# Kernel optimization log

Measured on AMD Instinct MI355X. Metric: run time of the kernel, lower is better.

The kernel has to match this reference:

```python
import jax, jax.numpy as jnp
import numpy as np

BIAS = 0.0001
TEMPERATURE = 1.0


def setup_inputs() -> dict:
    key = jax.random.key(0)
    k_h, k_w1, k_w2, k_u = jax.random.split(key, 4)
    N, H, Z = 8192, 64, 128
    h = jax.random.normal(k_h, (N, H), dtype=jnp.float32)
    W1 = jax.random.normal(k_w1, (H, H), dtype=jnp.float32) * (1.0 / np.sqrt(H))
    b1 = jnp.zeros((H,), dtype=jnp.float32)
    W2 = jax.random.normal(k_w2, (H, Z), dtype=jnp.float32) * (1.0 / np.sqrt(H))
    b2 = jnp.zeros((Z,), dtype=jnp.float32)
    noise_u = jax.random.uniform(k_u, (N, N), dtype=jnp.float32)
    return {"h": h, "W1": W1, "b1": b1, "W2": W2, "b2": b2, "noise_u": noise_u}


def reference(h, W1, b1, W2, b2, noise_u):
    # MLPA: Linear -> ReLU -> Linear, then outer-product adjacency logits
    Zmat = jnp.maximum(h @ W1 + b1, 0.0) @ W2 + b2          # [N, dim_z]
    adj_logits = Zmat @ Zmat.T                               # [N, N]
    # gumbel-sigmoid edge sampling (training path)
    eps = (2.0 * BIAS - 1.0) * noise_u + (1.0 - BIAS)        # uniform in [bias, 1-bias]
    gate = (jnp.log(eps) - jnp.log1p(-eps) + adj_logits) / TEMPERATURE
    adj = jax.nn.sigmoid(gate)
    # keep strict upper triangle, symmetrize
    adj = jnp.triu(adj, 1)
    adj = adj + adj.T
    # fill_diagonal_(1)
    N = adj.shape[0]
    idx = jnp.arange(N)
    adj = adj.at[idx, idx].set(1.0)
    # D^{-1/2} @ adj @ D^{-1/2} expressed as row/col rescale (same math)
    d = jnp.power(adj.sum(axis=1), -0.5)                     # [N]
    adj_norm = d[:, None] * adj * d[None, :]
    return adj_norm, adj_logits
```

## Files before the change

### kernel.cpp

```cpp
#include <hip/hip_runtime.h>
#include <hip/hip_bf16.h>
#include <math.h>

#define N 8192
#define ZD 128
#define NTILE 64
#define NUPPER 2080

typedef __attribute__((ext_vector_type(8))) _Float16 f16x8;
typedef __attribute__((ext_vector_type(4))) float f32x4;

__device__ __forceinline__ int tri_cum(int ti) {
    return (ti * (2 * NTILE + 1 - ti)) / 2;
}

__device__ __forceinline__ void tile_decode(int t, int& ti, int& tj) {
    int est = (int)((129.0f - sqrtf(16641.0f - 8.0f * (float)t)) * 0.5f);
    if (est < 0) est = 0;
    while (tri_cum(est) > t) --est;
    while (tri_cum(est + 1) <= t) ++est;
    ti = est;
    tj = est + (t - tri_cum(est));
}

__global__ __launch_bounds__(256) void k1_mlp(
    const float* __restrict__ h, const float* __restrict__ W1,
    const float* __restrict__ b1, const float* __restrict__ W2,
    const float* __restrict__ b2, _Float16* __restrict__ Zf,
    float* __restrict__ sums)
{
    __shared__ float W1s[64][65];
    __shared__ float W2s[64][129];
    __shared__ float hs[32][68];
    __shared__ float Ts[32][68];
    __shared__ float b1s[64];
    __shared__ float b2s[128];
    const int tid = threadIdx.x;
    const int row0 = blockIdx.x * 32;

    if (tid < 32) sums[row0 + tid] = 1.0f;

    for (int e = tid; e < 64 * 64; e += 256) W1s[e >> 6][e & 63] = W1[e];
    for (int e = tid; e < 64 * 128; e += 256) W2s[e >> 7][e & 127] = W2[e];
    for (int e = tid; e < 32 * 64; e += 256) hs[e >> 6][e & 63] = h[(size_t)row0 * 64 + e];
    if (tid < 64) b1s[tid] = b1[tid];
    if (tid < 128) b2s[tid] = b2[tid];
    __syncthreads();

    {
        const int c = tid & 63;
        const int r0 = (tid >> 6) * 8;
        float s[8];
        #pragma unroll
        for (int j = 0; j < 8; ++j) s[j] = b1s[c];
        #pragma unroll
        for (int k0 = 0; k0 < 64; k0 += 4) {
            const float w0 = W1s[k0 + 0][c], w1 = W1s[k0 + 1][c];
            const float w2 = W1s[k0 + 2][c], w3 = W1s[k0 + 3][c];
            #pragma unroll
            for (int j = 0; j < 8; ++j) {
                f32x4 hv = *(const f32x4*)&hs[r0 + j][k0];
                s[j] = fmaf(hv[0], w0, s[j]);
                s[j] = fmaf(hv[1], w1, s[j]);
                s[j] = fmaf(hv[2], w2, s[j]);
                s[j] = fmaf(hv[3], w3, s[j]);
            }
        }
        #pragma unroll
        for (int j = 0; j < 8; ++j) Ts[r0 + j][c] = fmaxf(s[j], 0.0f);
    }
    __syncthreads();

    {
        const int c = tid & 127;
        const int r0 = (tid >> 7) * 16;
        float s[16];
        #pragma unroll
        for (int j = 0; j < 16; ++j) s[j] = b2s[c];
        #pragma unroll
        for (int k0 = 0; k0 < 64; k0 += 4) {
            const float w0 = W2s[k0 + 0][c], w1 = W2s[k0 + 1][c];
            const float w2 = W2s[k0 + 2][c], w3 = W2s[k0 + 3][c];
            #pragma unroll
            for (int j = 0; j < 16; ++j) {
                f32x4 tv = *(const f32x4*)&Ts[r0 + j][k0];
                s[j] = fmaf(tv[0], w0, s[j]);
                s[j] = fmaf(tv[1], w1, s[j]);
                s[j] = fmaf(tv[2], w2, s[j]);
                s[j] = fmaf(tv[3], w3, s[j]);
            }
        }
        #pragma unroll
        for (int j = 0; j < 16; ++j)
            Zf[(size_t)(row0 + r0 + j) * ZD + c] = (_Float16)s[j];
    }
}

__global__ __launch_bounds__(256, 3) void k3_main(
    const _Float16* __restrict__ Zf, const float* __restrict__ noise,
    float* __restrict__ logits, unsigned char* __restrict__ vws,
    float* __restrict__ sums)
{
    int ti, tj;
    const int t = (blockIdx.x & 7) * (NUPPER / 8) + (blockIdx.x >> 3);
    tile_decode(t, ti, tj);
    const bool diag = (ti == tj);

    __shared__ float T[128][65];
    __shared__ float rs2[128][16];
    __shared__ float cs2[16][128];

    const int tid = threadIdx.x;
    const int lane = tid & 63;
    const int w = tid >> 6;
    const int wr = w >> 1, wc = w & 1;
    const int fr = lane & 15;
    const int kg = lane >> 4;
    const int i0 = ti * 128, j0 = tj * 128;

    unsigned char* __restrict__ vtile = vws + (size_t)t * (128 * 128);

    const _Float16* Ap = Zf + (size_t)(i0 + wr * 64) * ZD;
    const _Float16* Bp = Zf + (size_t)(j0 + wc * 64) * ZD;

    f32x4 acc[4][4];
    #pragma unroll
    for (int mf = 0; mf < 4; ++mf)
        #pragma unroll
        for (int nf = 0; nf < 4; ++nf)
            acc[mf][nf] = (f32x4)0.0f;

    #pragma unroll
    for (int kc = 0; kc < 4; ++kc) {
        const int ko = kc * 32 + kg * 8;
        f16x8 a[4], b[4];
        #pragma unroll
        for (int mf = 0; mf < 4; ++mf) {
            size_t off = (size_t)(mf * 16 + fr) * ZD + ko;
            a[mf] = *(const f16x8*)(Ap + off);
            b[mf] = *(const f16x8*)(Bp + off);
        }
        #pragma unroll
        for (int mf = 0; mf < 4; ++mf)
            #pragma unroll
            for (int nf = 0; nf < 4; ++nf)
                acc[mf][nf] = __builtin_amdgcn_mfma_f32_16x16x32_f16(a[mf], b[nf], acc[mf][nf], 0, 0, 0);
    }

    const int cid = tid & 15;
    const int c4 = cid * 4;
    const int rbase = tid >> 4;

    float rsacc[8];
    #pragma unroll
    for (int it = 0; it < 8; ++it) rsacc[it] = 0.0f;

    #pragma unroll
    for (int half = 0; half < 2; ++half) {
        __syncthreads();
        if (wc == half) {
            #pragma unroll
            for (int mf = 0; mf < 4; ++mf)
                #pragma unroll
                for (int nf = 0; nf < 4; ++nf)
                    #pragma unroll
                    for (int r = 0; r < 4; ++r)
                        T[wr * 64 + mf * 16 + (lane >> 4) * 4 + r][nf * 16 + fr] = acc[mf][nf][r];
        }
        __syncthreads();

        f32x4 csum = (f32x4)0.0f;
        #pragma unroll
        for (int it = 0; it < 8; ++it) {
            const int r = rbase + it * 16;
            f32x4 L4 = *(const f32x4*)&T[r][c4];
            const size_t g = (size_t)(i0 + r) * N + j0 + half * 64 + c4;
            __builtin_nontemporal_store(L4, (f32x4*)&logits[g]);
            f32x4 u4 = __builtin_nontemporal_load((const f32x4*)&noise[g]);
            float rsum = 0.0f;
            unsigned q = 0;
            #pragma unroll
            for (int e = 0; e < 4; ++e) {
                float u = u4[e];
                float eps = fmaf(-0.9998f, u, 0.9999f);
                float om  = fmaf( 0.9998f, u, 0.0001f);
                float ex = __expf(-L4[e]);
                float v = eps / fmaf(om, ex, eps);
                if (diag && r >= half * 64 + c4 + e) v = 0.0f;
                q |= ((unsigned)(int)rintf(v * 255.0f)) << (8 * e);
                rsum += v;
                csum[e] += v;
            }
            __builtin_nontemporal_store(q, (unsigned*)&vtile[r * 128 + half * 64 + c4]);
            rsacc[it] += rsum;
        }
        #pragma unroll
        for (int e = 0; e < 4; ++e)
            cs2[rbase][half * 64 + c4 + e] = csum[e];

        if (!diag) {
            #pragma unroll
            for (int it = 0; it < 8; ++it) {
                const int idx = tid + it * 256;
                const int c = idx >> 5;
                const int m4 = (idx & 31) * 4;
                f32x4 o;
                o[0] = T[m4 + 0][c]; o[1] = T[m4 + 1][c];
                o[2] = T[m4 + 2][c]; o[3] = T[m4 + 3][c];
                __builtin_nontemporal_store(o, (f32x4*)&logits[(size_t)(j0 + half * 64 + c) * N + i0 + m4]);
            }
        }
    }

    #pragma unroll
    for (int it = 0; it < 8; ++it)
        rs2[rbase + it * 16][cid] = rsacc[it];

    __syncthreads();

    if (tid < 128) {
        f32x4 a0 = *(const f32x4*)&rs2[tid][0];
        f32x4 a1 = *(const f32x4*)&rs2[tid][4];
        f32x4 a2 = *(const f32x4*)&rs2[tid][8];
        f32x4 a3 = *(const f32x4*)&rs2[tid][12];
        f32x4 s4 = a0 + a1 + a2 + a3;
        float rowsum = s4[0] + s4[1] + s4[2] + s4[3];
        float colsum = 0.0f;
        #pragma unroll
        for (int k = 0; k < 16; ++k) colsum += cs2[k][tid];
        if (diag) {
            atomicAdd(&sums[i0 + tid], rowsum + colsum);
        } else {
            atomicAdd(&sums[i0 + tid], rowsum);
            atomicAdd(&sums[j0 + tid], colsum);
        }
    }
}

__global__ __launch_bounds__(256, 4) void k5_norm(
    const unsigned char* __restrict__ vws, float* __restrict__ adj,
    const float* __restrict__ sums)
{
    int ti, tj;
    const int t = (blockIdx.x & 7) * (NUPPER / 8) + (blockIdx.x >> 3);
    tile_decode(t, ti, tj);
    const bool diag = (ti == tj);
    __shared__ float T[128][68];
    __shared__ float drow[128], dcol[128];
    const int tid = threadIdx.x;
    const int i0 = ti * 128, j0 = tj * 128;

    const unsigned char* __restrict__ vtile = vws + (size_t)t * (128 * 128);

    if (tid < 128) drow[tid] = rsqrtf(sums[i0 + tid]);
    else dcol[tid - 128] = rsqrtf(sums[j0 + tid - 128]);
    __syncthreads();

    const float inv255 = 1.0f / 255.0f;
    #pragma unroll 4
    for (int it = 0; it < 16; ++it) {
        int w = tid + it * 256;
        int m = w >> 5;
        int n4 = (w & 31) << 2;
        unsigned q = __builtin_nontemporal_load((const unsigned*)&vtile[m * 128 + n4]);
        float dm = drow[m];
        f32x4 o;
        o[0] = (float)(q & 255)         * inv255 * dm * dcol[n4 + 0];
        o[1] = (float)((q >> 8) & 255)  * inv255 * dm * dcol[n4 + 1];
        o[2] = (float)((q >> 16) & 255) * inv255 * dm * dcol[n4 + 2];
        o[3] = (float)(q >> 24)         * inv255 * dm * dcol[n4 + 3];
        __builtin_nontemporal_store(o, (f32x4*)&adj[(size_t)(i0 + m) * N + j0 + n4]);
        T[n4 + 0][m] = o[0]; T[n4 + 1][m] = o[1];
        T[n4 + 2][m] = o[2]; T[n4 + 3][m] = o[3];
    }
    __syncthreads();
    #pragma unroll 4
    for (int it = 0; it < 16; ++it) {
        int w = tid + it * 256;
        int c = w >> 5;
        int m4 = (w & 31) << 2;
        f32x4 o = *(const f32x4*)&T[c][m4];
        if (!diag) {
            __builtin_nontemporal_store(o, (f32x4*)&adj[(size_t)(j0 + c) * N + i0 + m4]);
        } else {
            #pragma unroll
            for (int e = 0; e < 4; ++e)
                if (m4 + e < c)
                    adj[(size_t)(j0 + c) * N + i0 + m4 + e] = o[e];
        }
    }
    if (diag && tid < 128) {
        float dm = drow[tid];
        adj[(size_t)(i0 + tid) * N + i0 + tid] = dm * dm;
    }
}

extern "C" void kernel_launch(void* const* d_in, const int* in_sizes, int n_in,
                              void* d_out, int out_size, void* d_ws, size_t ws_size,
                              hipStream_t stream)
{
    const float* h     = (const float*)d_in[0];
    const float* W1    = (const float*)d_in[1];
    const float* b1    = (const float*)d_in[2];
    const float* W2    = (const float*)d_in[3];
    const float* b2    = (const float*)d_in[4];
    const float* noise = (const float*)d_in[5];

    float* adj    = (float*)d_out;
    float* logits = adj + (size_t)N * N;

    _Float16* Zf       = (_Float16*)d_ws;
    unsigned char* vws = (unsigned char*)(Zf + (size_t)N * ZD);
    float* sums        = (float*)(vws + (size_t)NUPPER * 128 * 128);

    k1_mlp<<<256, 256, 0, stream>>>(h, W1, b1, W2, b2, Zf, sums);
    k3_main<<<NUPPER, 256, 0, stream>>>(Zf, noise, logits, vws, sums);
    k5_norm<<<NUPPER, 256, 0, stream>>>(vws, adj, sums);
}
```

Before: 213.7 us.

## Reduce row/column partial sums with wavefront shuffles to shrink LDS and raise occupancy

```diff
diff --git a/kernel.cpp b/kernel.cpp
--- a/kernel.cpp
+++ b/kernel.cpp
@@ -96,7 +96,7 @@
     }
 }
 
-__global__ __launch_bounds__(256, 3) void k3_main(
+__global__ __launch_bounds__(256, 4) void k3_main(
     const _Float16* __restrict__ Zf, const float* __restrict__ noise,
     float* __restrict__ logits, unsigned char* __restrict__ vws,
     float* __restrict__ sums)
@@ -107,8 +107,8 @@
     const bool diag = (ti == tj);
 
     __shared__ float T[128][65];
-    __shared__ float rs2[128][16];
-    __shared__ float cs2[16][128];
+    __shared__ float rs1[128];
+    __shared__ float cs2[4][128];
 
     const int tid = threadIdx.x;
     const int lane = tid & 63;
@@ -195,8 +195,13 @@
             rsacc[it] += rsum;
         }
         #pragma unroll
-        for (int e = 0; e < 4; ++e)
-            cs2[rbase][half * 64 + c4 + e] = csum[e];
+        for (int e = 0; e < 4; ++e) {
+            float cv = csum[e];
+            cv += __shfl_xor(cv, 16);
+            cv += __shfl_xor(cv, 32);
+            if (lane < 16)
+                cs2[w][half * 64 + lane * 4 + e] = cv;
+        }
 
         if (!diag) {
             #pragma unroll
@@ -213,21 +218,21 @@
     }
 
     #pragma unroll
-    for (int it = 0; it < 8; ++it)
-        rs2[rbase + it * 16][cid] = rsacc[it];
+    for (int it = 0; it < 8; ++it) {
+        float rv = rsacc[it];
+        rv += __shfl_xor(rv, 1);
+        rv += __shfl_xor(rv, 2);
+        rv += __shfl_xor(rv, 4);
+        rv += __shfl_xor(rv, 8);
+        if (cid == 0)
+            rs1[rbase + it * 16] = rv;
+    }
 
     __syncthreads();
 
     if (tid < 128) {
-        f32x4 a0 = *(const f32x4*)&rs2[tid][0];
-        f32x4 a1 = *(const f32x4*)&rs2[tid][4];
-        f32x4 a2 = *(const f32x4*)&rs2[tid][8];
-        f32x4 a3 = *(const f32x4*)&rs2[tid][12];
-        f32x4 s4 = a0 + a1 + a2 + a3;
-        float rowsum = s4[0] + s4[1] + s4[2] + s4[3];
-        float colsum = 0.0f;
-        #pragma unroll
-        for (int k = 0; k < 16; ++k) colsum += cs2[k][tid];
+        const float rowsum = rs1[tid];
+        const float colsum = cs2[0][tid] + cs2[1][tid] + cs2[2][tid] + cs2[3][tid];
         if (diag) {
             atomicAdd(&sums[i0 + tid], rowsum + colsum);
         } else {
```

Result: slower. 225.2 us (+5.4%).
